# Kernel optimization log

Hardware: AMD Instinct MI355X
Metric: run time of the kernel (lower is better)

## Reference

```python
import jax, jax.numpy as jnp
import numpy as np

S, B, F, D, DF, NH, FH = 1152, 2, 128, 1024, 2048, 8, 4
SEP = 1024
EPS = 1e-5

def ln(x, g, b):
    m = x.mean(-1, keepdims=True)
    v = ((x - m) ** 2).mean(-1, keepdims=True)
    return (x - m) * jax.lax.rsqrt(v + EPS) * g + b

def mha(q, k, v, wi, bi, wo, bo, nh):
    # torch MultiheadAttention, batch_first=False: inputs (L, N, E)
    E = q.shape[-1]
    hd = E // nh
    qh = (q @ wi[:E].T + bi[:E]).reshape(q.shape[0], -1, nh, hd)
    kh = (k @ wi[E:2 * E].T + bi[E:2 * E]).reshape(k.shape[0], -1, nh, hd)
    vh = (v @ wi[2 * E:].T + bi[2 * E:]).reshape(k.shape[0], -1, nh, hd)
    s = jnp.einsum('qnhd,knhd->nhqk', qh, kh) / jnp.sqrt(jnp.float32(hd))
    a = jax.nn.softmax(s, axis=-1)
    o = jnp.einsum('nhqk,knhd->qnhd', a, vh).reshape(q.shape[0], -1, E)
    return o @ wo.T + bo

def setup_inputs() -> dict:
    key = jax.random.key(0)
    it = iter(jax.random.split(key, 40))
    def p(shape, s=0.02):
        return jax.random.normal(next(it), shape, jnp.float32) * s
    z = lambda *sh: jnp.zeros(sh, jnp.float32)
    o = lambda *sh: jnp.ones(sh, jnp.float32)
    return dict(
        src=jax.random.normal(next(it), (S, B, F), jnp.float32),
        sep=SEP,
        sa_wi=p((3 * D, D)), sa_bi=z(3 * D), sa_wo=p((D, D)), sa_bo=z(D),
        fa_wi=p((3 * F, F)), fa_bi=z(3 * F), fa_wo=p((F, F)), fa_bo=z(F),
        pl1_w=p((F, 1)), pl1_b=z(F),
        pl2_w=p((DF, F)), pl2_b=z(DF),
        pl3_w=p((1, DF)), pl3_b=z(1),
        pl4_w=p((DF, F)), pl4_b=z(DF),
        pl5_w=p((D, DF)), pl5_b=z(D),
        pl6_w=p((DF, D)), pl6_b=z(DF),
        pl7_w=p((D, DF)), pl7_b=z(D),
        l1_w=p((DF, D)), l1_b=z(DF),
        l2_w=p((F, DF)), l2_b=z(F),
        pn1_g=o(F), pn1_b=z(F),
        pn2_g=o(D), pn2_b=z(D),
        n1_g=o(D), n1_b=z(D),
        n2_g=o(F), n2_b=z(F),
    )

def _forward(src, sa_wi, sa_bi, sa_wo, sa_bo, fa_wi, fa_bi, fa_wo, fa_bo,
             pl1_w, pl1_b, pl2_w, pl2_b, pl3_w, pl3_b, pl4_w, pl4_b,
             pl5_w, pl5_b, pl6_w, pl6_b, pl7_w, pl7_b, l1_w, l1_b, l2_w, l2_b,
             pn1_g, pn1_b, pn2_g, pn2_b, n1_g, n1_b, n2_g, n2_b, sep):
    Sn, Bn, Fn = src.shape
    relu = jax.nn.relu
    # feature-wise attention: 'b h w -> w (b h) 1'
    x = jnp.transpose(src, (2, 0, 1)).reshape(Fn, Sn * Bn, 1)
    x = x @ pl1_w.T + pl1_b                       # (F, S*B, emsize_f)
    x = mha(x, x, x, fa_wi, fa_bi, fa_wo, fa_bo, FH)
    x = relu(x @ pl2_w.T + pl2_b) @ pl3_w.T + pl3_b  # (F, S*B, 1)
    x = jnp.transpose(x.reshape(Fn, Sn, Bn), (1, 2, 0))  # 'w (b h) 1 -> b h w'
    src1 = ln(x + src, pn1_g, pn1_b)              # (S, B, F)
    src1_ = relu(src1 @ pl4_w.T + pl4_b) @ pl5_w.T + pl5_b  # (S, B, D)
    li = src1_[:sep]
    sl = mha(li, li, li, sa_wi, sa_bi, sa_wo, sa_bo, NH)
    sl = ln(sl + li, pn2_g, pn2_b)
    sl_ = relu(sl @ pl6_w.T + pl6_b) @ pl7_w.T + pl7_b
    sl_ = ln(sl_, pn2_g, pn2_b) + sl
    sr = mha(src1_[sep:], sl_, sl_, sa_wi, sa_bi, sa_wo, sa_bo, NH)
    src2 = jnp.concatenate([sl, sr], axis=0)      # (S, B, D)
    so = ln(src2 + src1_, n1_g, n1_b)
    ff = relu(so @ l1_w.T + l1_b) @ l2_w.T + l2_b  # (S, B, F)
    return ln(src1 + ff, n2_g, n2_b)

def reference(src, sa_wi, sa_bi, sa_wo, sa_bo, fa_wi, fa_bi, fa_wo, fa_bo,
              pl1_w, pl1_b, pl2_w, pl2_b, pl3_w, pl3_b, pl4_w, pl4_b,
              pl5_w, pl5_b, pl6_w, pl6_b, pl7_w, pl7_b, l1_w, l1_b, l2_w, l2_b,
              pn1_g, pn1_b, pn2_g, pn2_b, n1_g, n1_b, n2_g, n2_b, sep):
    return _forward(src, sa_wi, sa_bi, sa_wo, sa_bo, fa_wi, fa_bi, fa_wo, fa_bo,
                    pl1_w, pl1_b, pl2_w, pl2_b, pl3_w, pl3_b, pl4_w, pl4_b,
                    pl5_w, pl5_b, pl6_w, pl6_b, pl7_w, pl7_b, l1_w, l1_b,
                    l2_w, l2_b, pn1_g, pn1_b, pn2_g, pn2_b, n1_g, n1_b,
                    n2_g, n2_b, sep)
```

## Files before the change

kernel.cpp:

```cpp
#include <hip/hip_runtime.h>

using s16x8 = __attribute__((ext_vector_type(8))) short;
using f32x4 = __attribute__((ext_vector_type(4))) float;
using f32x2 = __attribute__((ext_vector_type(2))) float;
typedef unsigned short ushort_t;

__device__ __forceinline__ unsigned short f2bf(float f) {
    union { float f; unsigned u; } v; v.f = f;
    unsigned u = v.u + 0x7FFFu + ((v.u >> 16) & 1u);
    return (unsigned short)(u >> 16);
}
__device__ __forceinline__ float bf2f(unsigned short h) {
    union { unsigned u; float f; } v; v.u = ((unsigned)h) << 16;
    return v.f;
}

__device__ __forceinline__ float block_reduce(float v, int op, float* lds) {
    const int lane = threadIdx.x & 63;
    const int w    = threadIdx.x >> 6;
    const int nw   = blockDim.x >> 6;
#pragma unroll
    for (int off = 32; off > 0; off >>= 1) {
        float o = __shfl_down(v, off, 64);
        v = op ? fmaxf(v, o) : (v + o);
    }
    __syncthreads();
    if (lane == 0) lds[w] = v;
    __syncthreads();
    float r = lds[0];
    for (int i = 1; i < nw; i++) r = op ? fmaxf(r, lds[i]) : (r + lds[i]);
    return r;
}

__device__ __forceinline__ void load_lds16(const void* g, void* l) {
    __builtin_amdgcn_global_load_lds(
        (const __attribute__((address_space(1))) unsigned int*)g,
        (__attribute__((address_space(3))) unsigned int*)l, 16, 0, 0);
}

struct CvtArgs { const float* src[8]; ushort_t* dst[8]; int end[8]; };

__global__ __launch_bounds__(256)
void cvt_all(CvtArgs a)
{
    int i = blockIdx.x * 256 + threadIdx.x;
    int j = 0;
    while (j < 8 && i >= a.end[j]) j++;
    if (j >= 8) return;
    int li = i - (j ? a.end[j - 1] : 0);
    float4 v = *(const float4*)&a.src[j][(size_t)li * 4];
    ushort_t u[4] = { f2bf(v.x), f2bf(v.y), f2bf(v.z), f2bf(v.w) };
    *(uint2*)&a.dst[j][(size_t)li * 4] = *(uint2*)u;
}

template<bool RELU, bool SPLITK>
__global__ __launch_bounds__(256, 2)
void gemm_bf16(const ushort_t* __restrict__ A, const ushort_t* __restrict__ B,
               const float* __restrict__ bias, ushort_t* __restrict__ C,
               float* __restrict__ Cp, long pstride, int ksplen, int zmod,
               int M, int N, int K, int lda, int ldb, int ldc,
               long sAz, long sBz, long sCz, long sA2, long sB2, long sC2,
               int zshift, float alpha)
{
    __shared__ ushort_t As[128 * 32];
    __shared__ ushort_t Bs[128 * 32];

    const int tid = threadIdx.x;
    int zz = blockIdx.z;
    int ks = 0, z = zz;
    if (SPLITK) { ks = zz / zmod; z = zz - ks * zmod; }
    const int z1  = z & ((1 << zshift) - 1);
    const int z2  = z >> zshift;
    const int m0  = blockIdx.x * 128;
    const int n0  = blockIdx.y * 128;

    const ushort_t* Ab = A + (size_t)z1 * sAz + (size_t)z2 * sA2 + (size_t)m0 * lda;
    const ushort_t* Bb = B + (size_t)z1 * sBz + (size_t)z2 * sB2 + (size_t)n0 * ldb;

    const int wave = tid >> 6, lane = tid & 63;
    const int wm = (wave & 1) * 64, wn = (wave >> 1) * 64;
    const int mi = lane & 15, quad = lane >> 4;

    f32x4 acc[4][4];
#pragma unroll
    for (int i = 0; i < 4; i++)
#pragma unroll
        for (int j = 0; j < 4; j++) acc[i][j] = (f32x4)0.f;

    const int r_0 = tid >> 2,           g_0 = (tid & 3) ^ ((r_0 >> 1) & 3);
    const int r_1 = (tid + 256) >> 2,   g_1 = (tid & 3) ^ ((r_1 >> 1) & 3);

    const int kbeg = SPLITK ? ks * ksplen : 0;
    const int kend = SPLITK ? kbeg + ksplen : K;

    for (int k0 = kbeg; k0 < kend; k0 += 32) {
        load_lds16(Ab + (size_t)r_0 * lda + k0 + g_0 * 8, &As[tid * 8]);
        load_lds16(Ab + (size_t)r_1 * lda + k0 + g_1 * 8, &As[(tid + 256) * 8]);
        load_lds16(Bb + (size_t)r_0 * ldb + k0 + g_0 * 8, &Bs[tid * 8]);
        load_lds16(Bb + (size_t)r_1 * ldb + k0 + g_1 * 8, &Bs[(tid + 256) * 8]);
        __syncthreads();

        s16x8 af[4], bfr[4];
#pragma unroll
        for (int t = 0; t < 4; t++) {
            int r = wm + t * 16 + mi;
            af[t] = *(const s16x8*)&As[r * 32 + ((quad ^ ((r >> 1) & 3)) * 8)];
        }
#pragma unroll
        for (int t = 0; t < 4; t++) {
            int r = wn + t * 16 + mi;
            bfr[t] = *(const s16x8*)&Bs[r * 32 + ((quad ^ ((r >> 1) & 3)) * 8)];
        }
#pragma unroll
        for (int tm = 0; tm < 4; tm++)
#pragma unroll
            for (int tn = 0; tn < 4; tn++)
                acc[tm][tn] = __builtin_amdgcn_mfma_f32_16x16x32_bf16(af[tm], bfr[tn], acc[tm][tn], 0, 0, 0);
        __syncthreads();
    }

    if (SPLITK) {
        float* Cf = Cp + (size_t)ks * pstride + (size_t)z1 * sCz + (size_t)z2 * sC2;
#pragma unroll
        for (int tn = 0; tn < 4; tn++) {
            int col = n0 + wn + tn * 16 + mi;
#pragma unroll
            for (int tm = 0; tm < 4; tm++)
#pragma unroll
                for (int r = 0; r < 4; r++) {
                    int row = m0 + wm + tm * 16 + quad * 4 + r;
                    Cf[(size_t)row * ldc + col] = acc[tm][tn][r] * alpha;
                }
        }
    } else {
#pragma unroll
        for (int tn = 0; tn < 4; tn++) {
            int col = n0 + wn + tn * 16 + mi;
            float bv = bias ? bias[col] : 0.f;
#pragma unroll
            for (int tm = 0; tm < 4; tm++) {
#pragma unroll
                for (int r = 0; r < 4; r++) {
                    int row = m0 + wm + tm * 16 + quad * 4 + r;
                    float v = acc[tm][tn][r] * alpha + bv;
                    if (RELU) v = fmaxf(v, 0.f);
                    C[(size_t)z1 * sCz + (size_t)z2 * sC2 + (size_t)row * ldc + col] = f2bf(v);
                }
            }
        }
    }
}

template<bool RELU>
__global__ __launch_bounds__(256)
void sum_cvt(const float* __restrict__ parts, long pstride, int P,
             const float* __restrict__ bias, int ldc,
             ushort_t* __restrict__ out, int total4)
{
    int i = blockIdx.x * 256 + threadIdx.x;
    if (i >= total4) return;
    size_t idx = (size_t)i * 4;
    float4 s = *(const float4*)&parts[idx];
    for (int p = 1; p < P; p++) {
        float4 v = *(const float4*)&parts[(size_t)p * pstride + idx];
        s.x += v.x; s.y += v.y; s.z += v.z; s.w += v.w;
    }
    if (bias) {
        int col = (int)(idx % (size_t)ldc);
        s.x += bias[col]; s.y += bias[col + 1]; s.z += bias[col + 2]; s.w += bias[col + 3];
    }
    if (RELU) {
        s.x = fmaxf(s.x, 0.f); s.y = fmaxf(s.y, 0.f);
        s.z = fmaxf(s.z, 0.f); s.w = fmaxf(s.w, 0.f);
    }
    ushort_t u[4] = { f2bf(s.x), f2bf(s.y), f2bf(s.z), f2bf(s.w) };
    *(uint2*)&out[idx] = *(uint2*)u;
}

__global__ __launch_bounds__(256)
void sum_ln(const float* __restrict__ parts, long pstride, int P,
            const float* __restrict__ bias, const ushort_t* __restrict__ residB,
            const ushort_t* __restrict__ post, const float* __restrict__ g,
            const float* __restrict__ beta, ushort_t* __restrict__ out)
{
    __shared__ float red[4];
    const size_t row = blockIdx.x;
    const int tid = threadIdx.x;
    float xr[4];
    float s = 0.f, ss = 0.f;
#pragma unroll
    for (int i = 0; i < 4; i++) {
        int idx = i * 256 + tid;
        float x = bias[idx];
        for (int p = 0; p < P; p++) x += parts[(size_t)p * pstride + row * 1024 + idx];
        if (residB) x += bf2f(residB[row * 1024 + idx]);
        xr[i] = x; s += x; ss = fmaf(x, x, ss);
    }
    s  = block_reduce(s, 0, red);
    ss = block_reduce(ss, 0, red);
    float mean = s * (1.f / 1024.f);
    float var  = ss * (1.f / 1024.f) - mean * mean;
    float inv  = rsqrtf(var + 1e-5f);
#pragma unroll
    for (int i = 0; i < 4; i++) {
        int idx = i * 256 + tid;
        float v = (xr[i] - mean) * inv * g[idx] + beta[idx];
        if (post) v += bf2f(post[row * 1024 + idx]);
        out[row * 1024 + idx] = f2bf(v);
    }
}

__global__ __launch_bounds__(128)
void ln_part(const float* __restrict__ parts, long pstride, int P,
             const float* __restrict__ bias, const ushort_t* __restrict__ resid,
             const float* __restrict__ g, const float* __restrict__ beta,
             float* __restrict__ out)
{
    __shared__ float red[4];
    const int r = blockIdx.x, c = threadIdx.x;
    float x = bias[c] + bf2f(resid[r * 128 + c]);
    for (int p = 0; p < P; p++) x += parts[(size_t)p * pstride + (size_t)r * 128 + c];
    float s  = block_reduce(x, 0, red);
    float ss = block_reduce(x * x, 0, red);
    float mean = s * (1.f / 128.f);
    float var  = ss * (1.f / 128.f) - mean * mean;
    float inv  = rsqrtf(var + 1e-5f);
    out[(size_t)r * 128 + c] = (x - mean) * inv * g[c] + beta[c];
}

__global__ __launch_bounds__(256)
void transp128(const ushort_t* __restrict__ in, ushort_t* __restrict__ out,
               int ldin, long inz1, long inz2, long outz)
{
    __shared__ ushort_t T[64][136];
    const int z = blockIdx.z, z1 = z & 7, z2 = z >> 3;
    const int n0 = blockIdx.x * 64;
    const ushort_t* ip = in + (size_t)z1 * inz1 + (size_t)z2 * inz2;
    const int rr = threadIdx.x >> 2, cg = (threadIdx.x & 3) * 32;
#pragma unroll
    for (int c = 0; c < 4; c++) {
        s16x8 v = *(const s16x8*)(ip + (size_t)(n0 + rr) * ldin + cg + c * 8);
        *(s16x8*)&T[rr][cg + c * 8] = v;
    }
    __syncthreads();
    const int d = threadIdx.x >> 1, j0 = (threadIdx.x & 1) * 32;
    ushort_t* op = out + (size_t)z * outz + (size_t)d * 1024 + n0 + j0;
#pragma unroll
    for (int c = 0; c < 4; c++) {
        s16x8 v;
#pragma unroll
        for (int j = 0; j < 8; j++) v[j] = (short)T[j0 + c * 8 + j][d];
        *(s16x8*)(op + c * 8) = v;
    }
}

__global__ void precomp1(const float* __restrict__ fa_wi, const float* __restrict__ fa_bi,
                         const float* __restrict__ pl1_w, const float* __restrict__ pl1_b,
                         float* __restrict__ consts)
{
    int j = threadIdx.x;
    if (j < 384) {
        float u = 0.f, v = 0.f;
        for (int k = 0; k < 128; k++) {
            float w = fa_wi[j * 128 + k];
            u = fmaf(w, pl1_w[k], u);
            v = fmaf(w, pl1_b[k], v);
        }
        consts[j]       = u;
        consts[512 + j] = v + fa_bi[j];
    }
}

__global__ void precomp2(const float* __restrict__ fa_wo, const float* __restrict__ fa_bo,
                         float* __restrict__ consts)
{
    int tid = threadIdx.x;
    const float* u = consts;
    const float* v = consts + 512;
    if (tid < 16) {
        int h = tid >> 2, w = tid & 3;
        const float* ql = (w < 2) ? u : v;
        const float* kr = ((w & 1) == 0) ? u : v;
        float acc = 0.f;
        for (int d = 0; d < 32; d++) acc += ql[h * 32 + d] * kr[128 + h * 32 + d];
        consts[1024 + tid] = acc * 0.17677669529663687f;
    }
#pragma unroll
    for (int h = 0; h < 4; h++) {
        float acc = 0.f;
        for (int d = 0; d < 32; d++)
            acc = fmaf(fa_wo[tid * 128 + h * 32 + d], u[256 + h * 32 + d], acc);
        consts[1088 + h * 128 + tid] = acc;
    }
    float c0 = fa_bo[tid];
    for (int idx = 0; idx < 128; idx++)
        c0 = fmaf(fa_wo[tid * 128 + idx], v[256 + idx], c0);
    consts[1600 + tid] = c0;
}

__global__ void precomp3(const float* __restrict__ pl2_w, const float* __restrict__ pl2_b,
                         const float* __restrict__ consts, ushort_t* __restrict__ Gb)
{
    int m = blockIdx.x * 256 + threadIdx.x;
    const float* wv = consts + 1088;
    const float* c0 = consts + 1600;
    float a0 = 0.f, ah[4] = {0.f, 0.f, 0.f, 0.f};
    for (int j = 0; j < 128; j++) {
        float w = pl2_w[m * 128 + j];
        ah[0] = fmaf(w, wv[0 * 128 + j], ah[0]);
        ah[1] = fmaf(w, wv[1 * 128 + j], ah[1]);
        ah[2] = fmaf(w, wv[2 * 128 + j], ah[2]);
        ah[3] = fmaf(w, wv[3 * 128 + j], ah[3]);
        a0    = fmaf(w, c0[j], a0);
    }
    ushort_t row[8];
#pragma unroll
    for (int h = 0; h < 4; h++) row[h] = f2bf(ah[h]);
    row[4] = f2bf(a0 + pl2_b[m]);
    row[5] = row[6] = row[7] = 0;
    *(uint4*)&Gb[m * 8] = *(uint4*)row;
}

__global__ __launch_bounds__(128)
void feat_t(const float* __restrict__ src, const float* __restrict__ consts,
            ushort_t* __restrict__ Tp)
{
    __shared__ float sv[128];
    __shared__ float red[2];
    const int n = blockIdx.x, f = threadIdx.x;
    const float si = src[n * 128 + f];
    sv[f] = si;
    __syncthreads();

    float S1 = block_reduce(si, 0, red);
    float S2 = block_reduce(si * si, 0, red);
    float S3 = block_reduce(si * si * si, 0, red);
    float S4 = block_reduce(si * si * si * si, 0, red);
    float amax = block_reduce(fabsf(si), 1, red);

    float ph[4];
#pragma unroll
    for (int h = 0; h < 4; h++)
        ph[h] = consts[1024 + h * 4 + 0] * si + consts[1024 + h * 4 + 2];
    float pm = fmaxf(fmaxf(fabsf(ph[0]), fabsf(ph[1])), fmaxf(fabsf(ph[2]), fabsf(ph[3])));
    float pmax = block_reduce(pm, 1, red);

    ushort_t row[8];
    if (pmax * amax < 0.25f) {
#pragma unroll
        for (int h = 0; h < 4; h++) {
            float p = ph[h];
            float num = fmaf(p, fmaf(p, fmaf(p, S4 * (1.f / 6.f), 0.5f * S3), S2), S1);
            float den = fmaf(p, fmaf(p, fmaf(p, S3 * (1.f / 6.f), 0.5f * S2), S1), 128.f);
            row[h] = f2bf(num / den);
        }
    } else {
        float smax = block_reduce(si, 1, red);
        float smin = -block_reduce(-si, 1, red);
#pragma unroll
        for (int h = 0; h < 4; h++) {
            float p = ph[h];
            float m = fmaxf(p * smax, p * smin);
            float l = 0.f, t = 0.f;
            for (int j = 0; j < 128; j++) {
                float e = __expf(fmaf(p, sv[j], -m));
                l += e; t = fmaf(e, sv[j], t);
            }
            row[h] = f2bf(t / l);
        }
    }
    row[4] = 0x3F80;
    row[5] = row[6] = row[7] = 0;
    *(uint4*)&Tp[(size_t)(n * 128 + f) * 8] = *(uint4*)row;
}

__global__ __launch_bounds__(512)
void mlp_ln(const ushort_t* __restrict__ Tp, const float* __restrict__ src,
            const ushort_t* __restrict__ Gb, const float* __restrict__ pl3_w,
            const float* __restrict__ pl3_b, const float* __restrict__ pn1_g,
            const float* __restrict__ pn1_b, ushort_t* __restrict__ src1)
{
    __shared__ float ypart[512];
    __shared__ float red[8];

    const int n   = blockIdx.x;
    const int tid = threadIdx.x;

    const int wave = tid >> 6, lane = tid & 63;
    const int wm = (wave & 1) * 64;
    const int mq = wave >> 1;
    const int mi = lane & 15, quad = lane >> 4;

    s16x8 af[4];
#pragma unroll
    for (int t = 0; t < 4; t++) {
        s16x8 v = *(const s16x8*)&Tp[((size_t)n * 128 + wm + t * 16 + mi) * 8];
        af[t] = (quad == 0) ? v : (s16x8)0;
    }

    f32x2 partial2[4][2];
#pragma unroll
    for (int i = 0; i < 4; i++) { partial2[i][0] = (f32x2)0.f; partial2[i][1] = (f32x2)0.f; }
    const f32x2 zero2 = (f32x2)0.f;

#pragma unroll 4
    for (int mt = 0; mt < 32; mt++) {
        const int m0 = mq * 512 + mt * 16;
        s16x8 bfr = *(const s16x8*)&Gb[(size_t)(m0 + mi) * 8];
        float w = pl3_w[m0 + mi];
        f32x2 w2 = { w, w };
        f32x4 acc[4];
#pragma unroll
        for (int tm = 0; tm < 4; tm++)
            acc[tm] = __builtin_amdgcn_mfma_f32_16x16x32_bf16(af[tm], bfr, (f32x4)0.f, 0, 0, 0);
#pragma unroll
        for (int tm = 0; tm < 4; tm++) {
            f32x2* pa = (f32x2*)&acc[tm];
#pragma unroll
            for (int i = 0; i < 2; i++) {
                f32x2 r = __builtin_elementwise_max(pa[i], zero2);
                partial2[tm][i] = r * w2 + partial2[tm][i];
            }
        }
    }

#pragma unroll
    for (int tm = 0; tm < 4; tm++)
#pragma unroll
        for (int r = 0; r < 4; r++) {
            float v = partial2[tm][r >> 1][r & 1];
            v += __shfl_xor(v, 8);
            v += __shfl_xor(v, 4);
            v += __shfl_xor(v, 2);
            v += __shfl_xor(v, 1);
            if (mi == 0) ypart[mq * 128 + wm + tm * 16 + quad * 4 + r] = v;
        }
    __syncthreads();

    float yv = 0.f;
    const int f = tid & 127;
    if (tid < 128)
        yv = ypart[f] + ypart[128 + f] + ypart[256 + f] + ypart[384 + f]
           + pl3_b[0] + src[n * 128 + f];
    float s  = block_reduce(yv, 0, red);
    float ss = block_reduce(yv * yv, 0, red);
    float mean = s * (1.f / 128.f);
    float var  = ss * (1.f / 128.f) - mean * mean;
    float inv  = rsqrtf(var + 1e-5f);
    if (tid < 128)
        src1[n * 128 + f] = f2bf((yv - mean) * inv * pn1_g[f] + pn1_b[f]);
}

template<bool OUTF32>
__global__ void ln_bf16(const ushort_t* __restrict__ a, const ushort_t* __restrict__ b,
                        const ushort_t* __restrict__ post, const float* __restrict__ g,
                        const float* __restrict__ beta, void* __restrict__ out, int D)
{
    __shared__ float red[4];
    const size_t row = blockIdx.x;
    const int tid = threadIdx.x;
    const int nit = D / blockDim.x;
    const ushort_t* ap = a + row * D;
    const ushort_t* bp = b ? b + row * D : nullptr;
    float xr[4];
    float s = 0.f, ss = 0.f;
    for (int i = 0; i < nit; i++) {
        int idx = i * blockDim.x + tid;
        float x = bf2f(ap[idx]) + (bp ? bf2f(bp[idx]) : 0.f);
        xr[i] = x; s += x; ss = fmaf(x, x, ss);
    }
    s  = block_reduce(s, 0, red);
    ss = block_reduce(ss, 0, red);
    float mean = s / D, var = ss / D - mean * mean;
    float inv = rsqrtf(var + 1e-5f);
    const ushort_t* pp = post ? post + row * D : nullptr;
    for (int i = 0; i < nit; i++) {
        int idx = i * blockDim.x + tid;
        float v = (xr[i] - mean) * inv * g[idx] + beta[idx];
        if (pp) v += bf2f(pp[idx]);
        if (OUTF32) ((float*)out)[row * D + idx] = v;
        else        ((ushort_t*)out)[row * D + idx] = f2bf(v);
    }
}

__global__ __launch_bounds__(256)
void ln_cat2(const ushort_t* __restrict__ a1, const float* __restrict__ parts,
             long pstride, int P, const float* __restrict__ bias2, int split,
             const ushort_t* __restrict__ b, const float* __restrict__ g,
             const float* __restrict__ beta, ushort_t* __restrict__ out)
{
    __shared__ float red[4];
    const int row = blockIdx.x;
    const int tid = threadIdx.x;
    float xr[4];
    float s = 0.f, ss = 0.f;
#pragma unroll
    for (int i = 0; i < 4; i++) {
        int idx = i * 256 + tid;
        float x;
        if (row < split) {
            x = bf2f(a1[(size_t)row * 1024 + idx]);
        } else {
            int r2 = row - split;
            x = bias2[idx];
            for (int p = 0; p < P; p++)
                x += parts[(size_t)p * pstride + (size_t)r2 * 1024 + idx];
        }
        x += bf2f(b[(size_t)row * 1024 + idx]);
        xr[i] = x; s += x; ss = fmaf(x, x, ss);
    }
    s  = block_reduce(s, 0, red);
    ss = block_reduce(ss, 0, red);
    float mean = s * (1.f / 1024.f);
    float var  = ss * (1.f / 1024.f) - mean * mean;
    float inv  = rsqrtf(var + 1e-5f);
#pragma unroll
    for (int i = 0; i < 4; i++) {
        int idx = i * 256 + tid;
        out[(size_t)row * 1024 + idx] = f2bf((xr[i] - mean) * inv * g[idx] + beta[idx]);
    }
}

__global__ __launch_bounds__(256)
void softmax_bf16(ushort_t* __restrict__ S)
{
    __shared__ float red[4];
    const size_t row = blockIdx.x;
    ushort_t* p = S + row * 1024;
    const int tid = threadIdx.x;
    uint2 u = *(const uint2*)&p[tid * 4];
    ushort_t* us = (ushort_t*)&u;
    float xr[4];
    float mx = -3.4e38f;
#pragma unroll
    for (int i = 0; i < 4; i++) { xr[i] = bf2f(us[i]); mx = fmaxf(mx, xr[i]); }
    mx = block_reduce(mx, 1, red);
    float sum = 0.f;
#pragma unroll
    for (int i = 0; i < 4; i++) { xr[i] = __expf(xr[i] - mx); sum += xr[i]; }
    sum = block_reduce(sum, 0, red);
    float inv = 1.f / sum;
#pragma unroll
    for (int i = 0; i < 4; i++) us[i] = f2bf(xr[i] * inv);
    *(uint2*)&p[tid * 4] = u;
}

static inline void gemm_go(hipStream_t s, const ushort_t* A, const ushort_t* B,
                           const float* bias, ushort_t* C,
                           int M, int N, int K, int lda, int ldb, int ldc,
                           long sAz, long sBz, long sCz, int Z, float alpha,
                           bool relu,
                           long sA2 = 0, long sB2 = 0, long sC2 = 0, int zshift = 0,
                           int ksplit = 1, float* Cp = nullptr, long pstride = 0)
{
    dim3 g(M / 128, N / 128, Z * ksplit), b(256);
    int ksplen = K / ksplit;
    if (ksplit > 1)
        gemm_bf16<false, true ><<<g, b, 0, s>>>(A, B, nullptr, nullptr, Cp, pstride, ksplen, Z,
            M, N, K, lda, ldb, ldc, sAz, sBz, sCz, sA2, sB2, sC2, zshift, alpha);
    else if (relu)
        gemm_bf16<true,  false><<<g, b, 0, s>>>(A, B, bias, C, nullptr, 0, 0, Z,
            M, N, K, lda, ldb, ldc, sAz, sBz, sCz, sA2, sB2, sC2, zshift, alpha);
    else
        gemm_bf16<false, false><<<g, b, 0, s>>>(A, B, bias, C, nullptr, 0, 0, Z,
            M, N, K, lda, ldb, ldc, sAz, sBz, sCz, sA2, sB2, sC2, zshift, alpha);
}

extern "C" void kernel_launch(void* const* d_in, const int* in_sizes, int n_in,
                              void* d_out, int out_size, void* d_ws, size_t ws_size,
                              hipStream_t stream)
{
    const float* src   = (const float*)d_in[0];
    const float* sa_wi = (const float*)d_in[2];
    const float* sa_bi = (const float*)d_in[3];
    const float* sa_wo = (const float*)d_in[4];
    const float* sa_bo = (const float*)d_in[5];
    const float* fa_wi = (const float*)d_in[6];
    const float* fa_bi = (const float*)d_in[7];
    const float* fa_wo = (const float*)d_in[8];
    const float* fa_bo = (const float*)d_in[9];
    const float* pl1_w = (const float*)d_in[10];
    const float* pl1_b = (const float*)d_in[11];
    const float* pl2_w = (const float*)d_in[12];
    const float* pl2_b = (const float*)d_in[13];
    const float* pl3_w = (const float*)d_in[14];
    const float* pl3_b = (const float*)d_in[15];
    const float* pl4_w = (const float*)d_in[16];
    const float* pl4_b = (const float*)d_in[17];
    const float* pl5_w = (const float*)d_in[18];
    const float* pl5_b = (const float*)d_in[19];
    const float* pl6_w = (const float*)d_in[20];
    const float* pl6_b = (const float*)d_in[21];
    const float* pl7_w = (const float*)d_in[22];
    const float* pl7_b = (const float*)d_in[23];
    const float* l1_w  = (const float*)d_in[24];
    const float* l1_b  = (const float*)d_in[25];
    const float* l2_w  = (const float*)d_in[26];
    const float* l2_b  = (const float*)d_in[27];
    const float* pn1_g = (const float*)d_in[28];
    const float* pn1_b = (const float*)d_in[29];
    const float* pn2_g = (const float*)d_in[30];
    const float* pn2_b = (const float*)d_in[31];
    const float* n1_g  = (const float*)d_in[32];
    const float* n1_b  = (const float*)d_in[33];
    const float* n2_g  = (const float*)d_in[34];
    const float* n2_b  = (const float*)d_in[35];

    float* ws  = (float*)d_ws;
    float* out = (float*)d_out;

    float* CONSTS = ws;
    ushort_t* wsb = (ushort_t*)(ws + 16384);
    ushort_t* SAWIb  = wsb + 0;
    ushort_t* SAWOb  = wsb + 3145728;
    ushort_t* PL4b   = wsb + 4194304;
    ushort_t* PL5b   = wsb + 4456448;
    ushort_t* PL6b   = wsb + 6553600;
    ushort_t* PL7b   = wsb + 8650752;
    ushort_t* L1b    = wsb + 10747904;
    ushort_t* L2b    = wsb + 12845056;
    ushort_t* Gbb    = wsb + 13107200;
    ushort_t* SRC1b  = wsb + 13172736;
    ushort_t* HBIGb  = wsb + 13467648;
    ushort_t* SRC1_b = wsb + 18186240;
    ushort_t* QKVb   = wsb + 20545536;
    ushort_t* SBUFb  = wsb + 27623424;
    ushort_t* OBUFb  = wsb + 44400640;
    ushort_t* SLb    = wsb + 46497792;
    ushort_t* SLPb   = wsb + 48594944;
    ushort_t* SOb    = wsb + 50692096;
    ushort_t* TPb    = wsb + 53051392;
    float* PARTS = (float*)SBUFb;

    {
        CvtArgs a;
        const float* srcs[8] = { sa_wi, sa_wo, pl4_w, pl5_w, pl6_w, pl7_w, l1_w, l2_w };
        ushort_t*    dsts[8] = { SAWIb, SAWOb, PL4b, PL5b, PL6b, PL7b, L1b, L2b };
        int          ns[8]   = { 3145728, 1048576, 262144, 2097152, 2097152, 2097152, 2097152, 262144 };
        int cum = 0;
        for (int i = 0; i < 8; i++) { a.src[i] = srcs[i]; a.dst[i] = dsts[i]; cum += ns[i] / 4; a.end[i] = cum; }
        cvt_all<<<(cum + 255) / 256, 256, 0, stream>>>(a);
    }

    precomp1<<<1, 384, 0, stream>>>(fa_wi, fa_bi, pl1_w, pl1_b, CONSTS);
    precomp2<<<1, 128, 0, stream>>>(fa_wo, fa_bo, CONSTS);
    precomp3<<<8, 256, 0, stream>>>(pl2_w, pl2_b, CONSTS, Gbb);
    feat_t<<<2304, 128, 0, stream>>>(src, CONSTS, TPb);
    mlp_ln<<<2304, 512, 0, stream>>>(TPb, src, Gbb, pl3_w, pl3_b, pn1_g, pn1_b, SRC1b);

    gemm_go(stream, SRC1b, PL4b, pl4_b, HBIGb, 2304, 2048, 128, 128, 128, 2048, 0, 0, 0, 1, 1.f, true);
    gemm_go(stream, HBIGb, PL5b, nullptr, nullptr, 2304, 1024, 2048, 2048, 2048, 1024, 0, 0, 0, 1, 1.f, false,
            0, 0, 0, 0, 2, PARTS, 2359296);
    sum_cvt<false><<<2304, 256, 0, stream>>>(PARTS, 2359296, 2, pl5_b, 1024, SRC1_b, 589824);

    gemm_go(stream, SRC1_b, SAWIb, sa_bi, QKVb, 2304, 3072, 1024, 1024, 1024, 3072, 0, 0, 0, 1, 1.f, false);
    const float iscale = 0.08838834764831845f;
    ushort_t* VT1 = HBIGb;
    transp128<<<dim3(16, 1, 16), 256, 0, stream>>>(QKVb + 2048, VT1, 6144, 128, 3072, 131072);
    gemm_go(stream, QKVb, QKVb + 1024, nullptr, SBUFb,
            1024, 1024, 128, 6144, 6144, 1024, 128, 128, 1048576, 16, iscale, false,
            3072, 3072, 8388608, 3);
    softmax_bf16<<<16384, 256, 0, stream>>>(SBUFb);
    gemm_go(stream, SBUFb, VT1, nullptr, OBUFb,
            1024, 128, 1024, 1024, 1024, 2048, 1048576, 131072, 128, 16, 1.f, false,
            8388608, 1048576, 1024, 3);
    gemm_go(stream, OBUFb, SAWOb, nullptr, nullptr, 2048, 1024, 1024, 1024, 1024, 1024, 0, 0, 0, 1, 1.f, false,
            0, 0, 0, 0, 2, PARTS, 2097152);
    sum_ln<<<2048, 256, 0, stream>>>(PARTS, 2097152, 2, sa_bo, SRC1_b, nullptr, pn2_g, pn2_b, SLb);

    gemm_go(stream, SLb, PL6b, nullptr, nullptr, 2048, 2048, 1024, 1024, 1024, 2048, 0, 0, 0, 1, 1.f, false,
            0, 0, 0, 0, 2, PARTS, 4194304);
    sum_cvt<true><<<4096, 256, 0, stream>>>(PARTS, 4194304, 2, pl6_b, 2048, HBIGb, 1048576);
    gemm_go(stream, HBIGb, PL7b, nullptr, nullptr, 2048, 1024, 2048, 2048, 2048, 1024, 0, 0, 0, 1, 1.f, false,
            0, 0, 0, 0, 2, PARTS, 2097152);
    sum_ln<<<2048, 256, 0, stream>>>(PARTS, 2097152, 2, pl7_b, nullptr, SLb, pn2_g, pn2_b, SLPb);

    ushort_t* KV2 = SBUFb;
    ushort_t* S2  = SBUFb + 4456448;
    gemm_go(stream, SLPb, SAWIb + 1024 * 1024, sa_bi + 1024, KV2, 2048, 2048, 1024, 1024, 1024, 2048, 0, 0, 0, 1, 1.f, false);
    ushort_t* VT2 = HBIGb;
    transp128<<<dim3(16, 1, 16), 256, 0, stream>>>(KV2 + 1024, VT2, 4096, 128, 2048, 131072);
    gemm_go(stream, QKVb + 2048 * 3072, KV2, nullptr, S2,
            128, 1024, 128, 6144, 4096, 1024, 128, 128, 131072, 16, iscale, false,
            3072, 2048, 1048576, 3);
    softmax_bf16<<<2048, 256, 0, stream>>>(S2);
    gemm_go(stream, S2, VT2, nullptr, nullptr,
            128, 128, 1024, 1024, 1024, 2048, 131072, 131072, 128, 16, 1.f, false,
            1048576, 1048576, 1024, 3, 8, PARTS, 262144);
    sum_cvt<false><<<256, 256, 0, stream>>>(PARTS, 262144, 8, nullptr, 2048, OBUFb, 65536);
    gemm_go(stream, OBUFb, SAWOb, nullptr, nullptr, 256, 1024, 1024, 1024, 1024, 1024, 0, 0, 0, 1, 1.f, false,
            0, 0, 0, 0, 8, PARTS, 262144);

    ln_cat2<<<2304, 256, 0, stream>>>(SLb, PARTS, 262144, 8, sa_bo, 2048, SRC1_b, n1_g, n1_b, SOb);

    gemm_go(stream, SOb, L1b, nullptr, nullptr, 2304, 2048, 1024, 1024, 1024, 2048, 0, 0, 0, 1, 1.f, false,
            0, 0, 0, 0, 2, PARTS, 4718592);
    sum_cvt<true><<<4608, 256, 0, stream>>>(PARTS, 4718592, 2, l1_b, 2048, HBIGb, 1179648);
    gemm_go(stream, HBIGb, L2b, nullptr, nullptr, 2304, 128, 2048, 2048, 2048, 128, 0, 0, 0, 1, 1.f, false,
            0, 0, 0, 0, 8, PARTS, 294912);
    ln_part<<<2304, 128, 0, stream>>>(PARTS, 294912, 8, l2_b, SRC1b, n2_g, n2_b, out);
}
```

Baseline: 592.7 us.

## Deepen GEMM K-tile to 64, stage mlp_ln operands in LDS, merge precompute kernels

The bf16 GEMM now stages a K=64 slab per iteration with an 8-way XOR swizzle, which halves the number of barrier pairs per K and issues more MFMAs per sync. mlp_ln preloads the G table and pl3 weights into LDS and switches to 32x32x16 MFMA tiles, which cuts global reloads and shuffle-reduction work. precomp1 and precomp2 are merged into a single launch. The costs are doubled GEMM LDS use, which may lower occupancy, and a large LDS footprint per mlp_ln block.

```diff
diff --git a/kernel.cpp b/kernel.cpp
--- a/kernel.cpp
+++ b/kernel.cpp
@@ -1,8 +1,9 @@
 #include <hip/hip_runtime.h>
 
-using s16x8 = __attribute__((ext_vector_type(8))) short;
-using f32x4 = __attribute__((ext_vector_type(4))) float;
-using f32x2 = __attribute__((ext_vector_type(2))) float;
+using s16x8  = __attribute__((ext_vector_type(8))) short;
+using f32x4  = __attribute__((ext_vector_type(4))) float;
+using f32x16 = __attribute__((ext_vector_type(16))) float;
+using f32x2  = __attribute__((ext_vector_type(2))) float;
 typedef unsigned short ushort_t;
 
 __device__ __forceinline__ unsigned short f2bf(float f) {
@@ -62,8 +63,8 @@
                long sAz, long sBz, long sCz, long sA2, long sB2, long sC2,
                int zshift, float alpha)
 {
-    __shared__ ushort_t As[128 * 32];
-    __shared__ ushort_t Bs[128 * 32];
+    __shared__ ushort_t As[128 * 64];
+    __shared__ ushort_t Bs[128 * 64];
 
     const int tid = threadIdx.x;
     int zz = blockIdx.z;
@@ -87,35 +88,45 @@
 #pragma unroll
         for (int j = 0; j < 4; j++) acc[i][j] = (f32x4)0.f;
 
-    const int r_0 = tid >> 2,           g_0 = (tid & 3) ^ ((r_0 >> 1) & 3);
-    const int r_1 = (tid + 256) >> 2,   g_1 = (tid & 3) ^ ((r_1 >> 1) & 3);
+    int rs[4], gs[4];
+#pragma unroll
+    for (int p = 0; p < 4; p++) {
+        int ci = tid + p * 256;
+        rs[p] = ci >> 3;
+        gs[p] = (ci & 7) ^ (rs[p] & 7);
+    }
 
     const int kbeg = SPLITK ? ks * ksplen : 0;
     const int kend = SPLITK ? kbeg + ksplen : K;
 
-    for (int k0 = kbeg; k0 < kend; k0 += 32) {
-        load_lds16(Ab + (size_t)r_0 * lda + k0 + g_0 * 8, &As[tid * 8]);
-        load_lds16(Ab + (size_t)r_1 * lda + k0 + g_1 * 8, &As[(tid + 256) * 8]);
-        load_lds16(Bb + (size_t)r_0 * ldb + k0 + g_0 * 8, &Bs[tid * 8]);
-        load_lds16(Bb + (size_t)r_1 * ldb + k0 + g_1 * 8, &Bs[(tid + 256) * 8]);
+    for (int k0 = kbeg; k0 < kend; k0 += 64) {
+#pragma unroll
+        for (int p = 0; p < 4; p++)
+            load_lds16(Ab + (size_t)rs[p] * lda + k0 + gs[p] * 8, &As[(tid + p * 256) * 8]);
+#pragma unroll
+        for (int p = 0; p < 4; p++)
+            load_lds16(Bb + (size_t)rs[p] * ldb + k0 + gs[p] * 8, &Bs[(tid + p * 256) * 8]);
         __syncthreads();
 
-        s16x8 af[4], bfr[4];
-#pragma unroll
-        for (int t = 0; t < 4; t++) {
-            int r = wm + t * 16 + mi;
-            af[t] = *(const s16x8*)&As[r * 32 + ((quad ^ ((r >> 1) & 3)) * 8)];
-        }
-#pragma unroll
-        for (int t = 0; t < 4; t++) {
-            int r = wn + t * 16 + mi;
-            bfr[t] = *(const s16x8*)&Bs[r * 32 + ((quad ^ ((r >> 1) & 3)) * 8)];
-        }
-#pragma unroll
-        for (int tm = 0; tm < 4; tm++)
-#pragma unroll
-            for (int tn = 0; tn < 4; tn++)
-                acc[tm][tn] = __builtin_amdgcn_mfma_f32_16x16x32_bf16(af[tm], bfr[tn], acc[tm][tn], 0, 0, 0);
+#pragma unroll
+        for (int sub = 0; sub < 2; sub++) {
+            s16x8 af[4], bfr[4];
+#pragma unroll
+            for (int t = 0; t < 4; t++) {
+                int r = wm + t * 16 + mi;
+                af[t] = *(const s16x8*)&As[r * 64 + (((sub * 4 + quad) ^ (r & 7)) * 8)];
+            }
+#pragma unroll
+            for (int t = 0; t < 4; t++) {
+                int r = wn + t * 16 + mi;
+                bfr[t] = *(const s16x8*)&Bs[r * 64 + (((sub * 4 + quad) ^ (r & 7)) * 8)];
+            }
+#pragma unroll
+            for (int tm = 0; tm < 4; tm++)
+#pragma unroll
+                for (int tn = 0; tn < 4; tn++)
+                    acc[tm][tn] = __builtin_amdgcn_mfma_f32_16x16x32_bf16(af[tm], bfr[tn], acc[tm][tn], 0, 0, 0);
+        }
         __syncthreads();
     }
 
@@ -254,9 +265,10 @@
     }
 }
 
-__global__ void precomp1(const float* __restrict__ fa_wi, const float* __restrict__ fa_bi,
-                         const float* __restrict__ pl1_w, const float* __restrict__ pl1_b,
-                         float* __restrict__ consts)
+__global__ void precomp12(const float* __restrict__ fa_wi, const float* __restrict__ fa_bi,
+                          const float* __restrict__ pl1_w, const float* __restrict__ pl1_b,
+                          const float* __restrict__ fa_wo, const float* __restrict__ fa_bo,
+                          float* __restrict__ consts)
 {
     int j = threadIdx.x;
     if (j < 384) {
@@ -269,33 +281,30 @@
         consts[j]       = u;
         consts[512 + j] = v + fa_bi[j];
     }
-}
-
-__global__ void precomp2(const float* __restrict__ fa_wo, const float* __restrict__ fa_bo,
-                         float* __restrict__ consts)
-{
-    int tid = threadIdx.x;
-    const float* u = consts;
-    const float* v = consts + 512;
-    if (tid < 16) {
-        int h = tid >> 2, w = tid & 3;
-        const float* ql = (w < 2) ? u : v;
-        const float* kr = ((w & 1) == 0) ? u : v;
-        float acc = 0.f;
-        for (int d = 0; d < 32; d++) acc += ql[h * 32 + d] * kr[128 + h * 32 + d];
-        consts[1024 + tid] = acc * 0.17677669529663687f;
-    }
-#pragma unroll
-    for (int h = 0; h < 4; h++) {
-        float acc = 0.f;
-        for (int d = 0; d < 32; d++)
-            acc = fmaf(fa_wo[tid * 128 + h * 32 + d], u[256 + h * 32 + d], acc);
-        consts[1088 + h * 128 + tid] = acc;
-    }
-    float c0 = fa_bo[tid];
-    for (int idx = 0; idx < 128; idx++)
-        c0 = fmaf(fa_wo[tid * 128 + idx], v[256 + idx], c0);
-    consts[1600 + tid] = c0;
+    __syncthreads();
+    if (j < 128) {
+        const float* u = consts;
+        const float* v = consts + 512;
+        if (j < 16) {
+            int h = j >> 2, w = j & 3;
+            const float* ql = (w < 2) ? u : v;
+            const float* kr = ((w & 1) == 0) ? u : v;
+            float acc = 0.f;
+            for (int d = 0; d < 32; d++) acc += ql[h * 32 + d] * kr[128 + h * 32 + d];
+            consts[1024 + j] = acc * 0.17677669529663687f;
+        }
+#pragma unroll
+        for (int h = 0; h < 4; h++) {
+            float acc = 0.f;
+            for (int d = 0; d < 32; d++)
+                acc = fmaf(fa_wo[j * 128 + h * 32 + d], u[256 + h * 32 + d], acc);
+            consts[1088 + h * 128 + j] = acc;
+        }
+        float c0 = fa_bo[j];
+        for (int idx = 0; idx < 128; idx++)
+            c0 = fmaf(fa_wo[j * 128 + idx], v[256 + idx], c0);
+        consts[1600 + j] = c0;
+    }
 }
 
 __global__ void precomp3(const float* __restrict__ pl2_w, const float* __restrict__ pl2_b,
@@ -380,68 +389,69 @@
             const float* __restrict__ pl3_b, const float* __restrict__ pn1_g,
             const float* __restrict__ pn1_b, ushort_t* __restrict__ src1)
 {
-    __shared__ float ypart[512];
-    __shared__ float red[8];
+    __shared__ ushort_t Gs[2048 * 8];
+    __shared__ float    wlds[2048];
+    __shared__ float    ypart[2 * 128];
+    __shared__ float    red[8];
 
     const int n   = blockIdx.x;
     const int tid = threadIdx.x;
 
+#pragma unroll
+    for (int p = 0; p < 4; p++) {
+        int ci = tid + p * 512;
+        load_lds16(Gb + (size_t)ci * 8, &Gs[ci * 8]);
+    }
+    load_lds16(pl3_w + tid * 4, &wlds[tid * 4]);
+    __syncthreads();
+
     const int wave = tid >> 6, lane = tid & 63;
-    const int wm = (wave & 1) * 64;
-    const int mq = wave >> 1;
-    const int mi = lane & 15, quad = lane >> 4;
-
-    s16x8 af[4];
-#pragma unroll
-    for (int t = 0; t < 4; t++) {
-        s16x8 v = *(const s16x8*)&Tp[((size_t)n * 128 + wm + t * 16 + mi) * 8];
-        af[t] = (quad == 0) ? v : (s16x8)0;
-    }
-
-    f32x2 partial2[4][2];
-#pragma unroll
-    for (int i = 0; i < 4; i++) { partial2[i][0] = (f32x2)0.f; partial2[i][1] = (f32x2)0.f; }
+    const int f0   = (wave & 3) * 32;
+    const int mh   = wave >> 2;
+    const int c32  = lane & 31, half = lane >> 5;
+
+    s16x8 tv = *(const s16x8*)&Tp[((size_t)n * 128 + f0 + c32) * 8];
+    s16x8 af = half ? (s16x8)0 : tv;
+
+    f32x2 part[8];
+#pragma unroll
+    for (int i = 0; i < 8; i++) part[i] = (f32x2)0.f;
     const f32x2 zero2 = (f32x2)0.f;
 
 #pragma unroll 4
-    for (int mt = 0; mt < 32; mt++) {
-        const int m0 = mq * 512 + mt * 16;
-        s16x8 bfr = *(const s16x8*)&Gb[(size_t)(m0 + mi) * 8];
-        float w = pl3_w[m0 + mi];
+    for (int ct = 0; ct < 32; ct++) {
+        const int m0 = mh * 1024 + ct * 32;
+        s16x8 bfr = *(const s16x8*)&Gs[(m0 + c32) * 8];
+        float w = wlds[m0 + c32];
         f32x2 w2 = { w, w };
-        f32x4 acc[4];
-#pragma unroll
-        for (int tm = 0; tm < 4; tm++)
-            acc[tm] = __builtin_amdgcn_mfma_f32_16x16x32_bf16(af[tm], bfr, (f32x4)0.f, 0, 0, 0);
-#pragma unroll
-        for (int tm = 0; tm < 4; tm++) {
-            f32x2* pa = (f32x2*)&acc[tm];
-#pragma unroll
-            for (int i = 0; i < 2; i++) {
-                f32x2 r = __builtin_elementwise_max(pa[i], zero2);
-                partial2[tm][i] = r * w2 + partial2[tm][i];
-            }
-        }
-    }
-
-#pragma unroll
-    for (int tm = 0; tm < 4; tm++)
-#pragma unroll
-        for (int r = 0; r < 4; r++) {
-            float v = partial2[tm][r >> 1][r & 1];
-            v += __shfl_xor(v, 8);
-            v += __shfl_xor(v, 4);
-            v += __shfl_xor(v, 2);
-            v += __shfl_xor(v, 1);
-            if (mi == 0) ypart[mq * 128 + wm + tm * 16 + quad * 4 + r] = v;
-        }
+        f32x16 acc = __builtin_amdgcn_mfma_f32_32x32x16_bf16(af, bfr, (f32x16)0.f, 0, 0, 0);
+        f32x2* pa = (f32x2*)&acc;
+#pragma unroll
+        for (int i = 0; i < 8; i++) {
+            f32x2 r = __builtin_elementwise_max(pa[i], zero2);
+            part[i] = r * w2 + part[i];
+        }
+    }
+
+#pragma unroll
+    for (int reg = 0; reg < 16; reg++) {
+        float v = part[reg >> 1][reg & 1];
+        v += __shfl_xor(v, 1);
+        v += __shfl_xor(v, 2);
+        v += __shfl_xor(v, 4);
+        v += __shfl_xor(v, 8);
+        v += __shfl_xor(v, 16);
+        if (c32 == 0) {
+            int row = (reg & 3) + 8 * (reg >> 2) + 4 * half;
+            ypart[mh * 128 + f0 + row] = v;
+        }
+    }
     __syncthreads();
 
     float yv = 0.f;
     const int f = tid & 127;
     if (tid < 128)
-        yv = ypart[f] + ypart[128 + f] + ypart[256 + f] + ypart[384 + f]
-           + pl3_b[0] + src[n * 128 + f];
+        yv = ypart[f] + ypart[128 + f] + pl3_b[0] + src[n * 128 + f];
     float s  = block_reduce(yv, 0, red);
     float ss = block_reduce(yv * yv, 0, red);
     float mean = s * (1.f / 128.f);
@@ -642,8 +652,7 @@
         cvt_all<<<(cum + 255) / 256, 256, 0, stream>>>(a);
     }
 
-    precomp1<<<1, 384, 0, stream>>>(fa_wi, fa_bi, pl1_w, pl1_b, CONSTS);
-    precomp2<<<1, 128, 0, stream>>>(fa_wo, fa_bo, CONSTS);
+    precomp12<<<1, 384, 0, stream>>>(fa_wi, fa_bi, pl1_w, pl1_b, fa_wo, fa_bo, CONSTS);
     precomp3<<<8, 256, 0, stream>>>(pl2_w, pl2_b, CONSTS, Gbb);
     feat_t<<<2304, 128, 0, stream>>>(src, CONSTS, TPb);
     mlp_ln<<<2304, 512, 0, stream>>>(TPb, src, Gbb, pl3_w, pl3_b, pn1_g, pn1_b, SRC1b);
```

After: 550.4 us. -7.1%, faster.
